# Kernel tuning notes

Hardware: AMD Instinct MI355X
Metric: run time of the kernel (lower is better)

Reference implementation:

```python
import jax, jax.numpy as jnp
import numpy as np

BINS = 64
VMIN, VMAX = 0.0, 1.0


def _calc_histogram(x):
    # x: [B, C, H, W] float
    B, C, H, W = x.shape
    x_norm = jnp.clip((x - VMIN) / (VMAX - VMIN), 0.0, 1.0)
    flat = x_norm.reshape(B * C, H * W)
    # torch.histc semantics over [0,1]: bin i = [i/BINS, (i+1)/BINS), last bin closed.
    idx = jnp.clip((flat * BINS).astype(jnp.int32), 0, BINS - 1)  # [B*C, HW]
    row_offset = (jnp.arange(B * C, dtype=jnp.int32) * BINS)[:, None]
    flat_idx = (idx + row_offset).reshape(-1)
    counts = jax.ops.segment_sum(
        jnp.ones(flat_idx.shape, dtype=x.dtype), flat_idx,
        num_segments=B * C * BINS,
    ).reshape(B * C, BINS)
    counts = counts / jnp.clip(counts.sum(axis=1, keepdims=True), 1e-8, None)
    return counts.reshape(B, C, BINS)


def reference(fake_images, real_images):
    hist_fake = _calc_histogram(fake_images)
    hist_real = _calc_histogram(real_images)
    # loss_type == 'l1'
    return jnp.abs(hist_fake - hist_real).mean()


def setup_inputs() -> dict:
    key = jax.random.key(0)
    k1, k2 = jax.random.split(key)
    shape = (32, 3, 512, 512)
    fake_images = jax.random.uniform(k1, shape, dtype=jnp.float32)
    real_images = jax.random.uniform(k2, shape, dtype=jnp.float32)
    return {"fake_images": fake_images, "real_images": real_images}
```

## Files before the change

kernel.cpp:

```cpp
#include <hip/hip_runtime.h>


#define HW        262144
#define ROWS      96
#define NBINS     64
#define BPR       4
#define CHUNK     (HW / BPR)
#define THREADS   256
#define F4_ITERS  (CHUNK / 4 / THREADS)
#define NBLOCKS   (2 * ROWS * BPR)

typedef unsigned long long u64;

#define PROC4(v) do {                                                   \
    int b0 = min((int)((v).x * 64.0f), 63);                             \
    int b1 = min((int)((v).y * 64.0f), 63);                             \
    int b2 = min((int)((v).z * 64.0f), 63);                             \
    int b3 = min((int)((v).w * 64.0f), 63);                             \
    u64 m0 = 1ull << b0, m1 = 1ull << b1;                               \
    u64 m2 = 1ull << b2, m3 = 1ull << b3;                               \
    u64 s1 = m0 ^ m1, c1 = m0 & m1;                                     \
    u64 s2 = m2 ^ m3, c2 = m2 & m3;                                     \
    u64 S  = s1 ^ s2, C  = s1 & s2;                                     \
    u64 g0 = p0 & S;  p0 ^= S;                                          \
    u64 u  = c1 ^ c2, vv = c1 & c2;                                     \
    u64 s3 = u ^ C,   w  = u & C;                                       \
    u64 t3 = vv | w;                                                    \
    u64 t  = s3 ^ g0;                                                   \
    u64 g1 = (p1 & t) | (s3 & g0);  p1 ^= t;                            \
    u64 t2 = t3 ^ g1;                                                   \
    u64 g2 = (p2 & t2) | (t3 & g1); p2 ^= t2;                           \
    u64 g3 = p3 & g2; p3 ^= g2;                                         \
    u64 g4 = p4 & g3; p4 ^= g3;                                         \
    u64 g5 = p5 & g4; p5 ^= g4;                                         \
    u64 g6 = p6 & g5; p6 ^= g5;                                         \
    u64 g7 = p7 & g6; p7 ^= g6;                                         \
    p8 ^= g7;                                                           \
} while (0)

__global__ __launch_bounds__(THREADS, 3)
void hist_kernel(const float* __restrict__ fake,
                 const float* __restrict__ real,
                 unsigned int* __restrict__ partial) {
    __shared__ unsigned int bhist[NBINS];

    const int tid  = threadIdx.x;
    const int lane = tid & 63;

    if (tid < NBINS) bhist[tid] = 0u;
    __syncthreads();

    const int b     = blockIdx.x;
    const int chunk = b & (BPR - 1);
    const int rowg  = b >> 2;
    const float* src = (rowg < ROWS) ? fake : real;
    const int row    = (rowg < ROWS) ? rowg : (rowg - ROWS);

    const float4* __restrict__ q =
        (const float4*)(src + (size_t)row * HW + (size_t)chunk * CHUNK) + tid;

    u64 p0 = 0, p1 = 0, p2 = 0, p3 = 0, p4 = 0, p5 = 0, p6 = 0, p7 = 0, p8 = 0;

    float4 c0 = q[0 * THREADS];
    float4 c1 = q[1 * THREADS];
    float4 c2 = q[2 * THREADS];
    float4 c3 = q[3 * THREADS];
    for (int i = 4; i < F4_ITERS; i += 4) {
        float4 n0 = q[(i + 0) * THREADS];
        float4 n1 = q[(i + 1) * THREADS];
        float4 n2 = q[(i + 2) * THREADS];
        float4 n3 = q[(i + 3) * THREADS];
        PROC4(c0); PROC4(c1); PROC4(c2); PROC4(c3);
        c0 = n0; c1 = n1; c2 = n2; c3 = n3;
    }
    PROC4(c0); PROC4(c1); PROC4(c2); PROC4(c3);

    unsigned mycnt = 0;
#pragma unroll
    for (int bb = 0; bb < NBINS; ++bb) {
        unsigned ws =
              (unsigned)__popcll(__ballot((unsigned)((p0 >> bb) & 1ull)))
            + ((unsigned)__popcll(__ballot((unsigned)((p1 >> bb) & 1ull))) << 1)
            + ((unsigned)__popcll(__ballot((unsigned)((p2 >> bb) & 1ull))) << 2)
            + ((unsigned)__popcll(__ballot((unsigned)((p3 >> bb) & 1ull))) << 3)
            + ((unsigned)__popcll(__ballot((unsigned)((p4 >> bb) & 1ull))) << 4)
            + ((unsigned)__popcll(__ballot((unsigned)((p5 >> bb) & 1ull))) << 5)
            + ((unsigned)__popcll(__ballot((unsigned)((p6 >> bb) & 1ull))) << 6)
            + ((unsigned)__popcll(__ballot((unsigned)((p7 >> bb) & 1ull))) << 7)
            + ((unsigned)__popcll(__ballot((unsigned)((p8 >> bb) & 1ull))) << 8);
        if (lane == bb) mycnt = ws;
    }
    atomicAdd(&bhist[lane], mycnt);
    __syncthreads();

    if (tid < NBINS)
        partial[(size_t)b * NBINS + tid] = bhist[tid];
}

__global__ __launch_bounds__(256)
void loss1_kernel(const unsigned int* __restrict__ partial,
                  unsigned int* __restrict__ blocksum) {
    const int tid = threadIdx.x;
    const int g   = blockIdx.x * 256 + tid;
    const int r   = g >> 6;
    const int bb  = g & 63;
    unsigned cf = 0, cr = 0;
#pragma unroll
    for (int c = 0; c < BPR; ++c) {
        cf += partial[((r * BPR + c) * NBINS) + bb];
        cr += partial[(((ROWS + r) * BPR + c) * NBINS) + bb];
    }
    int d = (int)cf - (int)cr;
    int a = (d < 0) ? -d : d;
#pragma unroll
    for (int off = 32; off > 0; off >>= 1)
        a += __shfl_down(a, off, 64);
    __shared__ int wsum[4];
    if ((tid & 63) == 0) wsum[tid >> 6] = a;
    __syncthreads();
    if (tid == 0)
        blocksum[blockIdx.x] = (unsigned)(wsum[0] + wsum[1] + wsum[2] + wsum[3]);
}

__global__ __launch_bounds__(64)
void loss2_kernel(const unsigned int* __restrict__ blocksum,
                  float* __restrict__ out) {
    const int lane = threadIdx.x;
    int a = (lane < 24) ? (int)blocksum[lane] : 0;
#pragma unroll
    for (int off = 32; off > 0; off >>= 1)
        a += __shfl_down(a, off, 64);
    if (lane == 0)
        out[0] = (float)((double)a / (262144.0 * 6144.0));
}

extern "C" void kernel_launch(void* const* d_in, const int* in_sizes, int n_in,
                              void* d_out, int out_size, void* d_ws, size_t ws_size,
                              hipStream_t stream) {
    const float* fake = (const float*)d_in[0];
    const float* real = (const float*)d_in[1];
    unsigned int* partial  = (unsigned int*)d_ws;
    unsigned int* blocksum = partial + NBLOCKS * NBINS;
    float* out = (float*)d_out;

    hist_kernel<<<NBLOCKS, THREADS, 0, stream>>>(fake, real, partial);
    loss1_kernel<<<24, 256, 0, stream>>>(partial, blocksum);
    loss2_kernel<<<1, 64, 0, stream>>>(blocksum, out);
}
```

Measured before the change: 228.5 us.

## Split rows into more blocks and use an 8-deep register prefetch ring

```diff
diff --git a/kernel.cpp b/kernel.cpp
--- a/kernel.cpp
+++ b/kernel.cpp
@@ -4,11 +4,12 @@
 #define HW        262144
 #define ROWS      96
 #define NBINS     64
-#define BPR       4
+#define BPR       8
 #define CHUNK     (HW / BPR)
 #define THREADS   256
 #define F4_ITERS  (CHUNK / 4 / THREADS)
 #define NBLOCKS   (2 * ROWS * BPR)
+#define RING      8
 
 typedef unsigned long long u64;
 
@@ -34,11 +35,17 @@
     u64 g4 = p4 & g3; p4 ^= g3;                                         \
     u64 g5 = p5 & g4; p5 ^= g4;                                         \
     u64 g6 = p6 & g5; p6 ^= g5;                                         \
-    u64 g7 = p7 & g6; p7 ^= g6;                                         \
-    p8 ^= g7;                                                           \
+    p7 ^= g6;                                                           \
 } while (0)
 
-__global__ __launch_bounds__(THREADS, 3)
+#define STAGE(fk, idx) do {                                             \
+    float4 cur = fk;                                                    \
+    fk = q[(idx) * THREADS];                                            \
+    PROC4(cur);                                                         \
+    __builtin_amdgcn_sched_barrier(0);                                  \
+} while (0)
+
+__global__ __launch_bounds__(THREADS, 6)
 void hist_kernel(const float* __restrict__ fake,
                  const float* __restrict__ real,
                  unsigned int* __restrict__ partial) {
@@ -52,28 +59,38 @@
 
     const int b     = blockIdx.x;
     const int chunk = b & (BPR - 1);
-    const int rowg  = b >> 2;
+    const int rowg  = b >> 3;
     const float* src = (rowg < ROWS) ? fake : real;
     const int row    = (rowg < ROWS) ? rowg : (rowg - ROWS);
 
     const float4* __restrict__ q =
         (const float4*)(src + (size_t)row * HW + (size_t)chunk * CHUNK) + tid;
 
-    u64 p0 = 0, p1 = 0, p2 = 0, p3 = 0, p4 = 0, p5 = 0, p6 = 0, p7 = 0, p8 = 0;
+    u64 p0 = 0, p1 = 0, p2 = 0, p3 = 0, p4 = 0, p5 = 0, p6 = 0, p7 = 0;
 
-    float4 c0 = q[0 * THREADS];
-    float4 c1 = q[1 * THREADS];
-    float4 c2 = q[2 * THREADS];
-    float4 c3 = q[3 * THREADS];
-    for (int i = 4; i < F4_ITERS; i += 4) {
-        float4 n0 = q[(i + 0) * THREADS];
-        float4 n1 = q[(i + 1) * THREADS];
-        float4 n2 = q[(i + 2) * THREADS];
-        float4 n3 = q[(i + 3) * THREADS];
-        PROC4(c0); PROC4(c1); PROC4(c2); PROC4(c3);
-        c0 = n0; c1 = n1; c2 = n2; c3 = n3;
+    float4 f0 = q[0 * THREADS];
+    float4 f1 = q[1 * THREADS];
+    float4 f2 = q[2 * THREADS];
+    float4 f3 = q[3 * THREADS];
+    float4 f4 = q[4 * THREADS];
+    float4 f5 = q[5 * THREADS];
+    float4 f6 = q[6 * THREADS];
+    float4 f7 = q[7 * THREADS];
+    __builtin_amdgcn_sched_barrier(0);
+
+#pragma unroll 1
+    for (int i = RING; i <= F4_ITERS - RING; i += RING) {
+        STAGE(f0, i + 0);
+        STAGE(f1, i + 1);
+        STAGE(f2, i + 2);
+        STAGE(f3, i + 3);
+        STAGE(f4, i + 4);
+        STAGE(f5, i + 5);
+        STAGE(f6, i + 6);
+        STAGE(f7, i + 7);
     }
-    PROC4(c0); PROC4(c1); PROC4(c2); PROC4(c3);
+    PROC4(f0); PROC4(f1); PROC4(f2); PROC4(f3);
+    PROC4(f4); PROC4(f5); PROC4(f6); PROC4(f7);
 
     unsigned mycnt = 0;
 #pragma unroll
@@ -86,8 +103,7 @@
             + ((unsigned)__popcll(__ballot((unsigned)((p4 >> bb) & 1ull))) << 4)
             + ((unsigned)__popcll(__ballot((unsigned)((p5 >> bb) & 1ull))) << 5)
             + ((unsigned)__popcll(__ballot((unsigned)((p6 >> bb) & 1ull))) << 6)
-            + ((unsigned)__popcll(__ballot((unsigned)((p7 >> bb) & 1ull))) << 7)
-            + ((unsigned)__popcll(__ballot((unsigned)((p8 >> bb) & 1ull))) << 8);
+            + ((unsigned)__popcll(__ballot((unsigned)((p7 >> bb) & 1ull))) << 7);
         if (lane == bb) mycnt = ws;
     }
     atomicAdd(&bhist[lane], mycnt);
```

Result: slower. 252.1 us (+10.3%).
